# Performance work log

Measured on AMD Instinct MI355X. Metric: run time of the kernel, lower is better.

Reference implementation:

```python
import jax, jax.numpy as jnp
import numpy as np

IN, H, STEPS = 4, 64, 5

def setup_inputs() -> dict:
    key = jax.random.key(0)
    ks = jax.random.split(key, 12)
    s = 1.0 / np.sqrt(H)
    def u(k, shape):
        return jax.random.uniform(k, shape, jnp.float32, -s, s)
    return {
        "x":    jax.random.normal(ks[0], (4096, 512, IN), jnp.float32),
        "Wih0": u(ks[1], (4 * H, IN)),
        "Whh0": u(ks[2], (4 * H, H)),
        "bih0": u(ks[3], (4 * H,)),
        "bhh0": u(ks[4], (4 * H,)),
        "Wih1": u(ks[5], (4 * H, H)),
        "Whh1": u(ks[6], (4 * H, H)),
        "bih1": u(ks[7], (4 * H,)),
        "bhh1": u(ks[8], (4 * H,)),
        "Wfc":  u(ks[9], (IN * STEPS, H)),
        "bfc":  u(ks[10], (IN * STEPS,)),
    }

def _lstm_layer(x, Wih, Whh, bih, bhh, collect):
    # x: [B, T, in]; PyTorch gate order: i, f, g, o
    B = x.shape[0]
    xg = jnp.einsum('bti,gi->tbg', x, Wih) + bih  # precompute input gates [T,B,4H]
    h0 = jnp.zeros((B, H), x.dtype)
    c0 = jnp.zeros((B, H), x.dtype)

    def step(carry, xg_t):
        h, c = carry
        gates = xg_t + h @ Whh.T + bhh  # [B,4H]
        i, f, g, o = jnp.split(gates, 4, axis=-1)
        i = jax.nn.sigmoid(i); f = jax.nn.sigmoid(f)
        g = jnp.tanh(g);       o = jax.nn.sigmoid(o)
        c = f * c + i * g
        h = o * jnp.tanh(c)
        return (h, c), (h if collect else None)

    (h_last, _), ys = jax.lax.scan(step, (h0, c0), xg)
    return ys, h_last  # ys: [T,B,H] (or None)

def reference(x, Wih0, Whh0, bih0, bhh0, Wih1, Whh1, bih1, bhh1, Wfc, bfc):
    ys1, _ = _lstm_layer(x, Wih0, Whh0, bih0, bhh0, collect=True)   # [T,B,H]
    x2 = jnp.transpose(ys1, (1, 0, 2))                               # [B,T,H]
    _, h_last = _lstm_layer(x2, Wih1, Whh1, bih1, bhh1, collect=False)
    out = h_last @ Wfc.T + bfc                                       # [B, IN*STEPS]
    return out.reshape(-1, STEPS, IN)
```

## Files before the change

### kernel.cpp

```cpp
#include <hip/hip_runtime.h>
#include <cstdint>

#define BLOCK 512
#define BT 16
#define RS_H 136
#define RS_F 68

typedef __attribute__((ext_vector_type(8))) short bf16x8;
typedef __attribute__((ext_vector_type(4))) float f32x4;

#define LOG2E 1.44269504f

static __device__ __forceinline__ float exp2_fast(float x) {
#if __has_builtin(__builtin_amdgcn_exp2f)
    return __builtin_amdgcn_exp2f(x);
#else
    return __expf(x * 0.69314718056f);
#endif
}
static __device__ __forceinline__ float rcp_fast(float x) {
    return __builtin_amdgcn_rcpf(x);
}
static __device__ __forceinline__ unsigned short f2bf(float f) {
    union { float f; unsigned u; } v; v.f = f;
    unsigned r = v.u + 0x7fffu + ((v.u >> 16) & 1u);
    return (unsigned short)(r >> 16);
}
static __device__ __forceinline__ float sigm_y(float y) {
    return rcp_fast(1.0f + exp2_fast(y));
}
static __device__ __forceinline__ float tanh_y(float y) {
    return 1.0f - 2.0f * rcp_fast(exp2_fast(y) + 1.0f);
}
static __device__ __forceinline__ bf16x8 load_wfrag(const float* __restrict__ w, int off, float scale) {
    union { bf16x8 v; unsigned short s[8]; } u;
#pragma unroll
    for (int j = 0; j < 8; ++j) u.s[j] = f2bf(w[off + j] * scale);
    return u.v;
}

extern "C" __global__ void __launch_bounds__(BLOCK, 2)
lstm_fused3(const float* __restrict__ x,
            const float* __restrict__ Wih0, const float* __restrict__ Whh0,
            const float* __restrict__ bih0, const float* __restrict__ bhh0,
            const float* __restrict__ Wih1, const float* __restrict__ Whh1,
            const float* __restrict__ bih1, const float* __restrict__ bhh1,
            const float* __restrict__ Wfc,  const float* __restrict__ bfc,
            float* __restrict__ out)
{
    __shared__ unsigned short hbuf[2][BT * RS_H];
    __shared__ float hfin[BT * RS_F];

    const int tid   = threadIdx.x;
    const int b0    = blockIdx.x * BT;
    const int lane  = tid & 63;
    const int wv    = tid >> 6;
    const int layer = wv >> 2;
    const int cb    = (wv & 3) * 16;
    const int n16   = lane & 15;
    const int quad  = lane >> 4;

    for (int i = tid; i < 2 * BT * RS_H; i += BLOCK)
        ((unsigned short*)hbuf)[i] = 0;

    const float gsc[4] = {-LOG2E, -LOG2E, 2.0f * LOG2E, -LOG2E};

    bf16x8 wf[4][4];
    float bias[4];
    if (layer == 0) {
#pragma unroll
        for (int g = 0; g < 4; ++g) {
            const int gc = g * 64 + cb + n16;
            const float s = gsc[g];
            wf[g][0] = load_wfrag(Whh0 + gc * 64, quad * 8, s);
            wf[g][1] = load_wfrag(Whh0 + gc * 64, 32 + quad * 8, s);
            union { bf16x8 v; unsigned short s_[8]; } u;
#pragma unroll
            for (int c = 0; c < 4; ++c)
                u.s_[c] = (quad == 0) ? f2bf(Wih0[gc * 4 + c] * s) : (unsigned short)0;
            u.s_[4] = 0; u.s_[5] = 0; u.s_[6] = 0; u.s_[7] = 0;
            wf[g][2] = u.v;
            union { bf16x8 v; unsigned short s_[8]; } z;
#pragma unroll
            for (int c = 0; c < 8; ++c) z.s_[c] = 0;
            wf[g][3] = z.v;
            bias[g] = (bih0[gc] + bhh0[gc]) * s;
        }
    } else {
#pragma unroll
        for (int g = 0; g < 4; ++g) {
            const int gc = g * 64 + cb + n16;
            const float s = gsc[g];
            wf[g][0] = load_wfrag(Wih1 + gc * 64, quad * 8, s);
            wf[g][1] = load_wfrag(Wih1 + gc * 64, 32 + quad * 8, s);
            wf[g][2] = load_wfrag(Whh1 + gc * 64, quad * 8, s);
            wf[g][3] = load_wfrag(Whh1 + gc * 64, 32 + quad * 8, s);
            bias[g] = (bih1[gc] + bhh1[gc]) * s;
        }
    }

    float cst[4] = {0.f, 0.f, 0.f, 0.f};

    const f32x4* __restrict__ xrow = (const f32x4*)x + (size_t)(b0 + n16) * 512;
    f32x4 xnext = {0.f, 0.f, 0.f, 0.f};
    if (layer == 0) xnext = xrow[0];

    __syncthreads();

    for (int it = 0; it <= 512; ++it) {
        const unsigned short* rb = &hbuf[(it + 1) & 1][0];
        unsigned short*       wb = &hbuf[it & 1][0];

        const f32x4 xcur = xnext;
        if (layer == 0 && it < 511) xnext = xrow[it + 1];

        bf16x8 a0 = *(const bf16x8*)(rb + n16 * RS_H + quad * 8);
        bf16x8 a1 = *(const bf16x8*)(rb + n16 * RS_H + 32 + quad * 8);
        bf16x8 a2, a3;
        if (layer == 0) {
            union { bf16x8 v; unsigned short s[8]; } u;
            u.s[0] = (quad == 0) ? f2bf(xcur[0]) : (unsigned short)0;
            u.s[1] = (quad == 0) ? f2bf(xcur[1]) : (unsigned short)0;
            u.s[2] = (quad == 0) ? f2bf(xcur[2]) : (unsigned short)0;
            u.s[3] = (quad == 0) ? f2bf(xcur[3]) : (unsigned short)0;
            u.s[4] = 0; u.s[5] = 0; u.s[6] = 0; u.s[7] = 0;
            a2 = u.v;
            a3 = u.v;
        } else {
            a2 = *(const bf16x8*)(rb + n16 * RS_H + 64 + quad * 8);
            a3 = *(const bf16x8*)(rb + n16 * RS_H + 96 + quad * 8);
        }

        f32x4 acc[4];
#pragma unroll
        for (int g = 0; g < 4; ++g) {
            acc[g] = (f32x4){bias[g], bias[g], bias[g], bias[g]};
            acc[g] = __builtin_amdgcn_mfma_f32_16x16x32_bf16(a0, wf[g][0], acc[g], 0, 0, 0);
            acc[g] = __builtin_amdgcn_mfma_f32_16x16x32_bf16(a1, wf[g][1], acc[g], 0, 0, 0);
            acc[g] = __builtin_amdgcn_mfma_f32_16x16x32_bf16(a2, wf[g][2], acc[g], 0, 0, 0);
            acc[g] = __builtin_amdgcn_mfma_f32_16x16x32_bf16(a3, wf[g][3], acc[g], 0, 0, 0);
        }

        const bool active = layer ? (it >= 1) : (it < 512);
        if (active) {
#pragma unroll
            for (int r = 0; r < 4; ++r) {
                const float iv = sigm_y(acc[0][r]);
                const float fv = sigm_y(acc[1][r]);
                const float gv = tanh_y(acc[2][r]);
                const float ov = sigm_y(acc[3][r]);
                const float cc = fv * cst[r] + iv * gv;
                cst[r] = cc;
                const float hh = ov * tanh_y(cc * (2.0f * LOG2E));
                const int row = quad * 4 + r;
                wb[row * RS_H + layer * 64 + cb + n16] = f2bf(hh);
                if (layer == 1 && it == 512) hfin[row * RS_F + cb + n16] = hh;
            }
        }
        __syncthreads();
    }

    if (tid < BT * 20) {
        const int m = tid / 20, k = tid % 20;
        float acc = bfc[k];
#pragma unroll 8
        for (int j = 0; j < 64; ++j)
            acc += hfin[m * RS_F + j] * Wfc[k * 64 + j];
        out[(b0 + m) * 20 + k] = acc;
    }
}

extern "C" void kernel_launch(void* const* d_in, const int* in_sizes, int n_in,
                              void* d_out, int out_size, void* d_ws, size_t ws_size,
                              hipStream_t stream)
{
    (void)in_sizes; (void)n_in; (void)d_ws; (void)ws_size; (void)out_size;
    const float* xp    = (const float*)d_in[0];
    const float* Wih0p = (const float*)d_in[1];
    const float* Whh0p = (const float*)d_in[2];
    const float* bih0p = (const float*)d_in[3];
    const float* bhh0p = (const float*)d_in[4];
    const float* Wih1p = (const float*)d_in[5];
    const float* Whh1p = (const float*)d_in[6];
    const float* bih1p = (const float*)d_in[7];
    const float* bhh1p = (const float*)d_in[8];
    const float* Wfcp  = (const float*)d_in[9];
    const float* bfcp  = (const float*)d_in[10];

    lstm_fused3<<<dim3(256), dim3(BLOCK), 0, stream>>>(
        xp, Wih0p, Whh0p, bih0p, bhh0p, Wih1p, Whh1p, bih1p, bhh1p,
        Wfcp, bfcp, (float*)d_out);
}
```

Measured before the change: 508.4 us.

## Double block to 1024 threads, splitting gate activations across duplicated waves

The block grows to 16 waves: each layer/column-slice wave is duplicated, both copies compute the full MFMA gate tile, and each copy handles the nonlinearities and cell update for half of the rows. Layer 0 also drops its all-zero fourth MFMA. The aim is to halve the serial transcendental work per wave on the recurrent critical path and add latency hiding, at the cost of redundant MFMA work, more register pressure under the tighter launch bound, and a barrier across twice as many waves every step.

```diff
diff --git a/kernel.cpp b/kernel.cpp
--- a/kernel.cpp
+++ b/kernel.cpp
@@ -1,7 +1,7 @@
 #include <hip/hip_runtime.h>
 #include <cstdint>
 
-#define BLOCK 512
+#define BLOCK 1024
 #define BT 16
 #define RS_H 136
 #define RS_F 68
@@ -39,8 +39,8 @@
     return u.v;
 }
 
-extern "C" __global__ void __launch_bounds__(BLOCK, 2)
-lstm_fused3(const float* __restrict__ x,
+extern "C" __global__ void __launch_bounds__(BLOCK, 4)
+lstm_fused4(const float* __restrict__ x,
             const float* __restrict__ Wih0, const float* __restrict__ Whh0,
             const float* __restrict__ bih0, const float* __restrict__ bhh0,
             const float* __restrict__ Wih1, const float* __restrict__ Whh1,
@@ -55,7 +55,8 @@
     const int b0    = blockIdx.x * BT;
     const int lane  = tid & 63;
     const int wv    = tid >> 6;
-    const int layer = wv >> 2;
+    const int rh    = wv >> 3;
+    const int layer = (wv >> 2) & 1;
     const int cb    = (wv & 3) * 16;
     const int n16   = lane & 15;
     const int quad  = lane >> 4;
@@ -80,10 +81,6 @@
                 u.s_[c] = (quad == 0) ? f2bf(Wih0[gc * 4 + c] * s) : (unsigned short)0;
             u.s_[4] = 0; u.s_[5] = 0; u.s_[6] = 0; u.s_[7] = 0;
             wf[g][2] = u.v;
-            union { bf16x8 v; unsigned short s_[8]; } z;
-#pragma unroll
-            for (int c = 0; c < 8; ++c) z.s_[c] = 0;
-            wf[g][3] = z.v;
             bias[g] = (bih0[gc] + bhh0[gc]) * s;
         }
     } else {
@@ -99,7 +96,7 @@
         }
     }
 
-    float cst[4] = {0.f, 0.f, 0.f, 0.f};
+    float cst[2] = {0.f, 0.f};
 
     const f32x4* __restrict__ xrow = (const f32x4*)x + (size_t)(b0 + n16) * 512;
     f32x4 xnext = {0.f, 0.f, 0.f, 0.f};
@@ -116,7 +113,8 @@
 
         bf16x8 a0 = *(const bf16x8*)(rb + n16 * RS_H + quad * 8);
         bf16x8 a1 = *(const bf16x8*)(rb + n16 * RS_H + 32 + quad * 8);
-        bf16x8 a2, a3;
+
+        f32x4 acc[4];
         if (layer == 0) {
             union { bf16x8 v; unsigned short s[8]; } u;
             u.s[0] = (quad == 0) ? f2bf(xcur[0]) : (unsigned short)0;
@@ -124,38 +122,43 @@
             u.s[2] = (quad == 0) ? f2bf(xcur[2]) : (unsigned short)0;
             u.s[3] = (quad == 0) ? f2bf(xcur[3]) : (unsigned short)0;
             u.s[4] = 0; u.s[5] = 0; u.s[6] = 0; u.s[7] = 0;
-            a2 = u.v;
-            a3 = u.v;
+            const bf16x8 a2 = u.v;
+#pragma unroll
+            for (int g = 0; g < 4; ++g) {
+                acc[g] = (f32x4){bias[g], bias[g], bias[g], bias[g]};
+                acc[g] = __builtin_amdgcn_mfma_f32_16x16x32_bf16(a0, wf[g][0], acc[g], 0, 0, 0);
+                acc[g] = __builtin_amdgcn_mfma_f32_16x16x32_bf16(a1, wf[g][1], acc[g], 0, 0, 0);
+                acc[g] = __builtin_amdgcn_mfma_f32_16x16x32_bf16(a2, wf[g][2], acc[g], 0, 0, 0);
+            }
         } else {
-            a2 = *(const bf16x8*)(rb + n16 * RS_H + 64 + quad * 8);
-            a3 = *(const bf16x8*)(rb + n16 * RS_H + 96 + quad * 8);
-        }
-
-        f32x4 acc[4];
+            const bf16x8 a2 = *(const bf16x8*)(rb + n16 * RS_H + 64 + quad * 8);
+            const bf16x8 a3 = *(const bf16x8*)(rb + n16 * RS_H + 96 + quad * 8);
 #pragma unroll
-        for (int g = 0; g < 4; ++g) {
-            acc[g] = (f32x4){bias[g], bias[g], bias[g], bias[g]};
-            acc[g] = __builtin_amdgcn_mfma_f32_16x16x32_bf16(a0, wf[g][0], acc[g], 0, 0, 0);
-            acc[g] = __builtin_amdgcn_mfma_f32_16x16x32_bf16(a1, wf[g][1], acc[g], 0, 0, 0);
-            acc[g] = __builtin_amdgcn_mfma_f32_16x16x32_bf16(a2, wf[g][2], acc[g], 0, 0, 0);
-            acc[g] = __builtin_amdgcn_mfma_f32_16x16x32_bf16(a3, wf[g][3], acc[g], 0, 0, 0);
+            for (int g = 0; g < 4; ++g) {
+                acc[g] = (f32x4){bias[g], bias[g], bias[g], bias[g]};
+                acc[g] = __builtin_amdgcn_mfma_f32_16x16x32_bf16(a0, wf[g][0], acc[g], 0, 0, 0);
+                acc[g] = __builtin_amdgcn_mfma_f32_16x16x32_bf16(a1, wf[g][1], acc[g], 0, 0, 0);
+                acc[g] = __builtin_amdgcn_mfma_f32_16x16x32_bf16(a2, wf[g][2], acc[g], 0, 0, 0);
+                acc[g] = __builtin_amdgcn_mfma_f32_16x16x32_bf16(a3, wf[g][3], acc[g], 0, 0, 0);
+            }
         }
 
         const bool active = layer ? (it >= 1) : (it < 512);
         if (active) {
-#pragma unroll
-            for (int r = 0; r < 4; ++r) {
+            auto do_row = [&](int r, int cr) {
                 const float iv = sigm_y(acc[0][r]);
                 const float fv = sigm_y(acc[1][r]);
                 const float gv = tanh_y(acc[2][r]);
                 const float ov = sigm_y(acc[3][r]);
-                const float cc = fv * cst[r] + iv * gv;
-                cst[r] = cc;
+                const float cc = fv * cst[cr] + iv * gv;
+                cst[cr] = cc;
                 const float hh = ov * tanh_y(cc * (2.0f * LOG2E));
                 const int row = quad * 4 + r;
                 wb[row * RS_H + layer * 64 + cb + n16] = f2bf(hh);
                 if (layer == 1 && it == 512) hfin[row * RS_F + cb + n16] = hh;
-            }
+            };
+            if (rh == 0) { do_row(0, 0); do_row(1, 1); }
+            else         { do_row(2, 0); do_row(3, 1); }
         }
         __syncthreads();
     }
@@ -187,7 +190,7 @@
     const float* Wfcp  = (const float*)d_in[9];
     const float* bfcp  = (const float*)d_in[10];
 
-    lstm_fused3<<<dim3(256), dim3(BLOCK), 0, stream>>>(
+    lstm_fused4<<<dim3(256), dim3(BLOCK), 0, stream>>>(
         xp, Wih0p, Whh0p, bih0p, bhh0p, Wih1p, Whh1p, bih1p, bhh1p,
         Wfcp, bfcp, (float*)d_out);
 }
```

New measurement: 647.1 us. 27.3% more time.

## Replace block barriers with per-wave LDS progress flags between LSTM layers

Applied to the files above, without the earlier changes.

Replaces the per-timestep __syncthreads with spin-waits on LDS progress counters, one per wave for each layer. Layer 0 can run up to three steps ahead of layer 1 through a 4-deep h0 ring buffer, and layer 1 uses its own double buffer. Layer 0 also drops its all-zero fourth MFMA. The aim is to decouple the two layers and remove full-block barrier stalls. The cost is busy-wait polling of LDS and reliance on LDS ordering and volatile semantics for correctness.

```diff
diff --git a/kernel.cpp b/kernel.cpp
--- a/kernel.cpp
+++ b/kernel.cpp
@@ -3,7 +3,7 @@
 
 #define BLOCK 512
 #define BT 16
-#define RS_H 136
+#define HS 72
 #define RS_F 68
 
 typedef __attribute__((ext_vector_type(8))) short bf16x8;
@@ -39,8 +39,23 @@
     return u.v;
 }
 
+static __device__ __forceinline__ void spin_ge(volatile int* p, int target) {
+    if (target <= 0) return;
+    for (;;) {
+        int a = p[0], b = p[1], c = p[2], d = p[3];
+        int m0 = a < b ? a : b;
+        int m1 = c < d ? c : d;
+        if ((m0 < m1 ? m0 : m1) >= target) break;
+    }
+    __asm__ __volatile__("" ::: "memory");
+}
+static __device__ __forceinline__ void publish(volatile int* slot, int value, int lane) {
+    __asm__ __volatile__("s_waitcnt lgkmcnt(0)" ::: "memory");
+    if (lane == 0) *slot = value;
+}
+
 extern "C" __global__ void __launch_bounds__(BLOCK, 2)
-lstm_fused3(const float* __restrict__ x,
+lstm_fused7(const float* __restrict__ x,
             const float* __restrict__ Wih0, const float* __restrict__ Whh0,
             const float* __restrict__ bih0, const float* __restrict__ bhh0,
             const float* __restrict__ Wih1, const float* __restrict__ Whh1,
@@ -48,20 +63,24 @@
             const float* __restrict__ Wfc,  const float* __restrict__ bfc,
             float* __restrict__ out)
 {
-    __shared__ unsigned short hbuf[2][BT * RS_H];
+    __shared__ unsigned short h0buf[4][BT * HS];
+    __shared__ unsigned short h1buf[2][BT * HS];
     __shared__ float hfin[BT * RS_F];
+    __shared__ int prog0[4];
+    __shared__ int prog1[4];
 
     const int tid   = threadIdx.x;
     const int b0    = blockIdx.x * BT;
     const int lane  = tid & 63;
     const int wv    = tid >> 6;
     const int layer = wv >> 2;
-    const int cb    = (wv & 3) * 16;
+    const int cw    = wv & 3;
+    const int cb    = cw * 16;
     const int n16   = lane & 15;
     const int quad  = lane >> 4;
 
-    for (int i = tid; i < 2 * BT * RS_H; i += BLOCK)
-        ((unsigned short*)hbuf)[i] = 0;
+    for (int i = tid; i < BT * HS; i += BLOCK) { h0buf[3][i] = 0; h1buf[1][i] = 0; }
+    if (tid < 4) { prog0[tid] = 0; prog1[tid] = 0; }
 
     const float gsc[4] = {-LOG2E, -LOG2E, 2.0f * LOG2E, -LOG2E};
 
@@ -80,10 +99,6 @@
                 u.s_[c] = (quad == 0) ? f2bf(Wih0[gc * 4 + c] * s) : (unsigned short)0;
             u.s_[4] = 0; u.s_[5] = 0; u.s_[6] = 0; u.s_[7] = 0;
             wf[g][2] = u.v;
-            union { bf16x8 v; unsigned short s_[8]; } z;
-#pragma unroll
-            for (int c = 0; c < 8; ++c) z.s_[c] = 0;
-            wf[g][3] = z.v;
             bias[g] = (bih0[gc] + bhh0[gc]) * s;
         }
     } else {
@@ -107,42 +122,70 @@
 
     __syncthreads();
 
-    for (int it = 0; it <= 512; ++it) {
-        const unsigned short* rb = &hbuf[(it + 1) & 1][0];
-        unsigned short*       wb = &hbuf[it & 1][0];
-
-        const f32x4 xcur = xnext;
-        if (layer == 0 && it < 511) xnext = xrow[it + 1];
-
-        bf16x8 a0 = *(const bf16x8*)(rb + n16 * RS_H + quad * 8);
-        bf16x8 a1 = *(const bf16x8*)(rb + n16 * RS_H + 32 + quad * 8);
-        bf16x8 a2, a3;
-        if (layer == 0) {
-            union { bf16x8 v; unsigned short s[8]; } u;
-            u.s[0] = (quad == 0) ? f2bf(xcur[0]) : (unsigned short)0;
-            u.s[1] = (quad == 0) ? f2bf(xcur[1]) : (unsigned short)0;
-            u.s[2] = (quad == 0) ? f2bf(xcur[2]) : (unsigned short)0;
-            u.s[3] = (quad == 0) ? f2bf(xcur[3]) : (unsigned short)0;
-            u.s[4] = 0; u.s[5] = 0; u.s[6] = 0; u.s[7] = 0;
-            a2 = u.v;
-            a3 = u.v;
-        } else {
-            a2 = *(const bf16x8*)(rb + n16 * RS_H + 64 + quad * 8);
-            a3 = *(const bf16x8*)(rb + n16 * RS_H + 96 + quad * 8);
-        }
-
-        f32x4 acc[4];
-#pragma unroll
-        for (int g = 0; g < 4; ++g) {
-            acc[g] = (f32x4){bias[g], bias[g], bias[g], bias[g]};
-            acc[g] = __builtin_amdgcn_mfma_f32_16x16x32_bf16(a0, wf[g][0], acc[g], 0, 0, 0);
-            acc[g] = __builtin_amdgcn_mfma_f32_16x16x32_bf16(a1, wf[g][1], acc[g], 0, 0, 0);
-            acc[g] = __builtin_amdgcn_mfma_f32_16x16x32_bf16(a2, wf[g][2], acc[g], 0, 0, 0);
-            acc[g] = __builtin_amdgcn_mfma_f32_16x16x32_bf16(a3, wf[g][3], acc[g], 0, 0, 0);
-        }
-
-        const bool active = layer ? (it >= 1) : (it < 512);
-        if (active) {
+    if (layer == 0) {
+        for (int s = 0; s < 512; ++s) {
+            spin_ge(prog0, s);
+            spin_ge(prog1, s - 3);
+
+            const f32x4 xcur = xnext;
+            if (s < 511) xnext = xrow[s + 1];
+
+            const unsigned short* rb = h0buf[(s + 3) & 3];
+            bf16x8 a0 = *(const bf16x8*)(rb + n16 * HS + quad * 8);
+            bf16x8 a1 = *(const bf16x8*)(rb + n16 * HS + 32 + quad * 8);
+            union { bf16x8 v; unsigned short s_[8]; } u;
+            u.s_[0] = (quad == 0) ? f2bf(xcur[0]) : (unsigned short)0;
+            u.s_[1] = (quad == 0) ? f2bf(xcur[1]) : (unsigned short)0;
+            u.s_[2] = (quad == 0) ? f2bf(xcur[2]) : (unsigned short)0;
+            u.s_[3] = (quad == 0) ? f2bf(xcur[3]) : (unsigned short)0;
+            u.s_[4] = 0; u.s_[5] = 0; u.s_[6] = 0; u.s_[7] = 0;
+            const bf16x8 a2 = u.v;
+
+            f32x4 acc[4];
+#pragma unroll
+            for (int g = 0; g < 4; ++g) {
+                acc[g] = (f32x4){bias[g], bias[g], bias[g], bias[g]};
+                acc[g] = __builtin_amdgcn_mfma_f32_16x16x32_bf16(a0, wf[g][0], acc[g], 0, 0, 0);
+                acc[g] = __builtin_amdgcn_mfma_f32_16x16x32_bf16(a1, wf[g][1], acc[g], 0, 0, 0);
+                acc[g] = __builtin_amdgcn_mfma_f32_16x16x32_bf16(a2, wf[g][2], acc[g], 0, 0, 0);
+            }
+
+            unsigned short* wb = h0buf[s & 3];
+#pragma unroll
+            for (int r = 0; r < 4; ++r) {
+                const float iv = sigm_y(acc[0][r]);
+                const float fv = sigm_y(acc[1][r]);
+                const float gv = tanh_y(acc[2][r]);
+                const float ov = sigm_y(acc[3][r]);
+                const float cc = fv * cst[r] + iv * gv;
+                cst[r] = cc;
+                wb[(quad * 4 + r) * HS + cb + n16] = f2bf(ov * tanh_y(cc * (2.0f * LOG2E)));
+            }
+            publish(&prog0[cw], s + 1, lane);
+        }
+    } else {
+        for (int s = 0; s < 512; ++s) {
+            spin_ge(prog0, s + 1);
+            spin_ge(prog1, s);
+
+            const unsigned short* rb0 = h0buf[s & 3];
+            const unsigned short* rb1 = h1buf[(s + 1) & 1];
+            bf16x8 a0 = *(const bf16x8*)(rb0 + n16 * HS + quad * 8);
+            bf16x8 a1 = *(const bf16x8*)(rb0 + n16 * HS + 32 + quad * 8);
+            bf16x8 a2 = *(const bf16x8*)(rb1 + n16 * HS + quad * 8);
+            bf16x8 a3 = *(const bf16x8*)(rb1 + n16 * HS + 32 + quad * 8);
+
+            f32x4 acc[4];
+#pragma unroll
+            for (int g = 0; g < 4; ++g) {
+                acc[g] = (f32x4){bias[g], bias[g], bias[g], bias[g]};
+                acc[g] = __builtin_amdgcn_mfma_f32_16x16x32_bf16(a0, wf[g][0], acc[g], 0, 0, 0);
+                acc[g] = __builtin_amdgcn_mfma_f32_16x16x32_bf16(a1, wf[g][1], acc[g], 0, 0, 0);
+                acc[g] = __builtin_amdgcn_mfma_f32_16x16x32_bf16(a2, wf[g][2], acc[g], 0, 0, 0);
+                acc[g] = __builtin_amdgcn_mfma_f32_16x16x32_bf16(a3, wf[g][3], acc[g], 0, 0, 0);
+            }
+
+            unsigned short* wb = h1buf[s & 1];
 #pragma unroll
             for (int r = 0; r < 4; ++r) {
                 const float iv = sigm_y(acc[0][r]);
@@ -153,12 +196,14 @@
                 cst[r] = cc;
                 const float hh = ov * tanh_y(cc * (2.0f * LOG2E));
                 const int row = quad * 4 + r;
-                wb[row * RS_H + layer * 64 + cb + n16] = f2bf(hh);
-                if (layer == 1 && it == 512) hfin[row * RS_F + cb + n16] = hh;
-            }
-        }
-        __syncthreads();
-    }
+                wb[row * HS + cb + n16] = f2bf(hh);
+                if (s == 511) hfin[row * RS_F + cb + n16] = hh;
+            }
+            publish(&prog1[cw], s + 1, lane);
+        }
+    }
+
+    __syncthreads();
 
     if (tid < BT * 20) {
         const int m = tid / 20, k = tid % 20;
@@ -187,7 +232,7 @@
     const float* Wfcp  = (const float*)d_in[9];
     const float* bfcp  = (const float*)d_in[10];
 
-    lstm_fused3<<<dim3(256), dim3(BLOCK), 0, stream>>>(
+    lstm_fused7<<<dim3(256), dim3(BLOCK), 0, stream>>>(
         xp, Wih0p, Whh0p, bih0p, bhh0p, Wih1p, Whh1p, bih1p, bhh1p,
         Wfcp, bfcp, (float*)d_out);
 }
```

Result: slower. 622.4 us (+22.4%).
